# Kernel tuning notes

Measured on AMD Instinct MI355X. Metric: run time of the kernel, lower is better.

Reference implementation:

```python
import jax, jax.numpy as jnp
import numpy as np

VOCAB = 32000
EMB = 256
HID = 512
BATCH = 32
MAXLEN = 64
START_TOKEN = 0


def setup_inputs() -> dict:
    key = jax.random.key(0)
    ks = jax.random.split(key, 10)
    return {
        "encoder_outputs": jax.random.normal(ks[0], (BATCH, 64, HID), dtype=jnp.float32),
        "encoder_hidden": jax.random.normal(ks[1], (1, BATCH, HID), dtype=jnp.float32),
        "target_tensor": jax.random.randint(ks[2], (BATCH, MAXLEN), 0, VOCAB),
        "embedding": jax.random.normal(ks[3], (VOCAB, EMB), dtype=jnp.float32) * 0.02,
        "W_ih": jax.random.normal(ks[4], (3 * HID, EMB), dtype=jnp.float32) * 0.05,
        "W_hh": jax.random.normal(ks[5], (3 * HID, HID), dtype=jnp.float32) * 0.05,
        "b_ih": jax.random.normal(ks[6], (3 * HID,), dtype=jnp.float32) * 0.05,
        "b_hh": jax.random.normal(ks[7], (3 * HID,), dtype=jnp.float32) * 0.05,
        "W_out": jax.random.normal(ks[8], (VOCAB, HID), dtype=jnp.float32) * 0.05,
        "b_out": jax.random.normal(ks[9], (VOCAB,), dtype=jnp.float32) * 0.05,
    }


def _gru_scan(x_seq, h0, W_ih, W_hh, b_ih, b_hh):
    # x_seq: [T, B, E]; h0: [B, H]. torch nn.GRU gate math/order (r, z, n).
    def step(h, x):
        gi = x @ W_ih.T + b_ih            # [B, 3H]
        gh = h @ W_hh.T + b_hh            # [B, 3H]
        i_r, i_z, i_n = jnp.split(gi, 3, axis=-1)
        h_r, h_z, h_n = jnp.split(gh, 3, axis=-1)
        r = jax.nn.sigmoid(i_r + h_r)
        z = jax.nn.sigmoid(i_z + h_z)
        n = jnp.tanh(i_n + r * h_n)
        h_new = (1.0 - z) * n + z * h
        return h_new, h_new
    hT, ys = jax.lax.scan(step, h0, x_seq)
    return ys, hT


def reference(encoder_outputs, encoder_hidden, target_tensor, embedding,
              W_ih, W_hh, b_ih, b_hh, W_out, b_out):
    B = encoder_outputs.shape[0]
    # Teacher forcing: step 0 consumes START, step i consumes target[:, i-1].
    start = jnp.full((B, 1), START_TOKEN, dtype=target_tensor.dtype)
    dec_in = jnp.concatenate([start, target_tensor[:, :-1]], axis=1)  # [B, T]
    # embed -> (dropout p=0 is identity) -> relu
    emb = jax.nn.relu(embedding[dec_in])                # [B, T, E]
    x_seq = jnp.swapaxes(emb, 0, 1)                     # [T, B, E]
    h0 = encoder_hidden[0]                              # [B, H] (num_layers=1)
    ys, hT = _gru_scan(x_seq, h0, W_ih, W_hh, b_ih, b_hh)  # ys: [T, B, H]
    hidden_seq = jnp.swapaxes(ys, 0, 1)                 # [B, T, H]
    logits = jnp.einsum("bth,vh->btv", hidden_seq, W_out) + b_out  # [B, T, V]
    log_probs = jax.nn.log_softmax(logits, axis=-1)
    decoder_hidden = hT[None]                           # [1, B, H]
    return log_probs, decoder_hidden
```

## Files before the change

### kernel.cpp

```cpp
#include <hip/hip_runtime.h>
#include <hip/hip_bf16.h>
#include <math.h>


typedef __bf16 bf16x8 __attribute__((ext_vector_type(8)));
typedef float  f32x4  __attribute__((ext_vector_type(4)));
typedef unsigned short u16;
typedef u16 u16x8v __attribute__((ext_vector_type(8)));
typedef u16 u16x4v __attribute__((ext_vector_type(4)));

#define BTV (32L * 64 * 32000)

#define OFF_X    (0L)
#define SZ_X     (2048L * 256 * 2)
#define OFF_WIH  (OFF_X + SZ_X)
#define SZ_WIH   (1536L * 256 * 2)
#define OFF_WHH  (OFF_WIH + SZ_WIH)
#define SZ_WHH   (1536L * 512 * 2)
#define OFF_WOUT (OFF_WHH + SZ_WHH)
#define SZ_WOUT  (32000L * 512 * 2)
#define OFF_GI   (OFF_WOUT + SZ_WOUT)
#define SZ_GI    (2048L * 1536 * 4)
#define OFF_HS   (OFF_GI + SZ_GI)
#define SZ_HS    (2048L * 512 * 2)
#define OFF_HB   (OFF_HS + SZ_HS)
#define SZ_HB    (2L * 32 * 512 * 2)
#define OFF_FLG  (OFF_HB + SZ_HB)
#define SZ_FLG   (512L)
#define OFF_EV   (OFF_FLG + SZ_FLG)
#define SZ_EV    (64L)
#define WS_NEED  (OFF_EV + SZ_EV)
#define OFF_LG   (WS_NEED + 4096 - (WS_NEED % 4096))
#define SZ_LG    (2048L * 32000 * 2)
#define WS_BIG   (OFF_LG + SZ_LG)

__device__ __forceinline__ u16 f2bf(float f) {
  union { float f; unsigned u; } a; a.f = f;
  unsigned r = a.u + 0x7fffu + ((a.u >> 16) & 1u);
  return (u16)(r >> 16);
}

__device__ __forceinline__ float bf2f(u16 u) {
  union { unsigned u; float f; } a; a.u = ((unsigned)u) << 16;
  return a.f;
}

__device__ __forceinline__ void gload16(const void* g, void* l) {
  __builtin_amdgcn_global_load_lds(
      (const __attribute__((address_space(1))) unsigned int*)g,
      (__attribute__((address_space(3))) unsigned int*)l, 16, 0, 0);
}

extern "C" __global__ void k_cast(const float* __restrict__ s, u16* __restrict__ d, int n4) {
  int i = blockIdx.x * blockDim.x + threadIdx.x;
  int st = gridDim.x * blockDim.x;
  for (; i < n4; i += st) {
    float4 v = reinterpret_cast<const float4*>(s)[i];
    u16x4v o; o.x = f2bf(v.x); o.y = f2bf(v.y); o.z = f2bf(v.z); o.w = f2bf(v.w);
    reinterpret_cast<u16x4v*>(d)[i] = o;
  }
}

extern "C" __global__ void k_embed(const float* __restrict__ emb, const int* __restrict__ tgt,
                                   u16* __restrict__ X) {
  int idx = blockIdx.x * 256 + threadIdx.x;
  int row = idx >> 5;
  int c8  = (idx & 31) << 3;
  int t = row >> 5, b = row & 31;
  int token = (t == 0) ? 0 : tgt[b * 64 + t - 1];
  const float* e = emb + (long)token * 256 + c8;
  u16x8v o;
#pragma unroll
  for (int i = 0; i < 8; ++i) { float v = e[i]; o[i] = f2bf(v > 0.f ? v : 0.f); }
  *reinterpret_cast<u16x8v*>(X + (long)row * 256 + c8) = o;
}

extern "C" __global__ void k_init(unsigned* flags, unsigned* evars) {
  int i = threadIdx.x;
  if (i < 128) {
    unsigned z = 0u;
    asm volatile("global_store_dword %0, %1, off sc0 sc1"
                 :: "v"(flags + i), "v"(z) : "memory");
  }
  if (i < 10) atomicExch(&evars[i], i == 8 ? 0xFFFFFFFFu : 0u);
}

template <bool BF16OUT>
__global__ void __launch_bounds__(256)
k_gemm_t(const u16* __restrict__ A, const u16* __restrict__ B,
         const float* __restrict__ bias, float* __restrict__ C,
         u16* __restrict__ C2, int M, int N, int K) {
  __shared__ u16 At[128 * 32];
  __shared__ u16 Bt[128 * 32];
  int mt = M >> 7;
  int bn = blockIdx.x / mt, bm = blockIdx.x % mt;
  int tid = threadIdx.x, wave = tid >> 6, lane = tid & 63;
  int wr = wave >> 1, wc = wave & 1;
  f32x4 acc[4][4] = {};
  const u16* ga = A + (long)(bm * 128 + wave * 32 + (lane >> 2)) * K + ((lane & 3) << 3);
  const u16* gb = B + (long)(bn * 128 + wave * 32 + (lane >> 2)) * K + ((lane & 3) << 3);
  u16* la0 = &At[wave * 1024]; u16* la1 = la0 + 512;
  u16* lb0 = &Bt[wave * 1024]; u16* lb1 = lb0 + 512;
  long k16 = 16L * K;
  for (int k0 = 0; k0 < K; k0 += 32) {
    if (k0) __syncthreads();
    gload16(ga + k0, la0);
    gload16(ga + k16 + k0, la1);
    gload16(gb + k0, lb0);
    gload16(gb + k16 + k0, lb1);
    __syncthreads();
    bf16x8 af[4], bfr[4];
#pragma unroll
    for (int mi = 0; mi < 4; ++mi)
      af[mi] = *reinterpret_cast<const bf16x8*>(
          &At[(wr * 64 + mi * 16 + (lane & 15)) * 32 + ((lane >> 4) << 3)]);
#pragma unroll
    for (int ni = 0; ni < 4; ++ni)
      bfr[ni] = *reinterpret_cast<const bf16x8*>(
          &Bt[(wc * 64 + ni * 16 + (lane & 15)) * 32 + ((lane >> 4) << 3)]);
#pragma unroll
    for (int mi = 0; mi < 4; ++mi)
#pragma unroll
      for (int ni = 0; ni < 4; ++ni)
        acc[mi][ni] = __builtin_amdgcn_mfma_f32_16x16x32_bf16(af[mi], bfr[ni], acc[mi][ni], 0, 0, 0);
  }
  int rb = bm * 128 + wr * 64 + ((lane >> 4) << 2);
  int cb = bn * 128 + wc * 64 + (lane & 15);
#pragma unroll
  for (int mi = 0; mi < 4; ++mi)
#pragma unroll
    for (int ni = 0; ni < 4; ++ni) {
      int col = cb + ni * 16;
      float bv = bias[col];
#pragma unroll
      for (int q = 0; q < 4; ++q) {
        int rr = rb + mi * 16 + q;
        if (BF16OUT) C2[(long)rr * N + col] = f2bf(acc[mi][ni][q] + bv);
        else         C[(long)rr * N + col] = acc[mi][ni][q] + bv;
      }
    }
}

extern "C" __global__ void __launch_bounds__(768, 1)
k_gru5(const float* __restrict__ gi, const u16* __restrict__ Whh,
       const float* __restrict__ bhh, const float* __restrict__ eh,
       u16* __restrict__ Hb, u16* __restrict__ HS, float* __restrict__ outH,
       unsigned* flags, unsigned* evars) {
  __shared__ u16 Ah[32 * 512];
  __shared__ float gh[3][32][65];
  __shared__ int role_s;
  int tid = threadIdx.x, wave = tid >> 6, lane = tid & 63;
  if (tid == 0) {
    unsigned xcc;
    asm volatile("s_getreg_b32 %0, hwreg(20, 0, 32)" : "=s"(xcc));
    xcc &= 7u;
    unsigned arr = atomicAdd(&evars[xcc], 1u);
    if (arr == 7u) atomicCAS(&evars[8], 0xFFFFFFFFu, xcc);
    unsigned L = 0xFFFFFFFFu;
    for (int it = 0; it < (1 << 24) && L == 0xFFFFFFFFu; ++it) {
      asm volatile("global_load_dword %0, %1, off sc0 sc1\n\ts_waitcnt vmcnt(0)"
                   : "=v"(L) : "v"(evars + 8) : "memory");
    }
    int role = -1;
    if (L == xcc) {
      unsigned c = atomicAdd(&evars[9], 1u);
      if (c < 8u) role = (int)c;
    }
    role_s = role;
  }
  __syncthreads();
  int g = role_s;
  if (g < 0) return;
  int j0 = g * 64;
  int gate = wave >> 2;
  int uh = (wave >> 1) & 1;
  int sig = wave & 1;
  bf16x8 barr[2][8];
  {
    const u16* wbase = Whh + (long)(gate * 512 + j0 + uh * 32) * 512 + sig * 256;
#pragma unroll
    for (int ut = 0; ut < 2; ++ut)
#pragma unroll
      for (int kt = 0; kt < 8; ++kt)
        barr[ut][kt] = *reinterpret_cast<const bf16x8*>(
            wbase + (long)(ut * 16 + (lane & 15)) * 512 + kt * 32 + ((lane >> 4) << 3));
  }
  float hprev[3] = {0.f, 0.f, 0.f}, bb0[3] = {}, bb1[3] = {}, bb2[3] = {};
#pragma unroll
  for (int s = 0; s < 3; ++s) {
    int o = s * 768 + tid;
    if (o < 2048) {
      int b = o >> 6, u = o & 63, j = j0 + u;
      hprev[s] = eh[b * 512 + j];
      bb0[s] = bhh[j]; bb1[s] = bhh[512 + j]; bb2[s] = bhh[1024 + j];
    }
  }
  for (int t = 0; t < 64; ++t) {
    int cur = t & 1, nxt = cur ^ 1;
    float grv[3] = {}, gzv[3] = {}, gnv[3] = {};
#pragma unroll
    for (int s = 0; s < 3; ++s) {
      int o = s * 768 + tid;
      if (o < 2048) {
        int b = o >> 6, u = o & 63, j = j0 + u;
        const float* gp = gi + ((long)t * 32 + b) * 1536;
        grv[s] = gp[j]; gzv[s] = gp[512 + j]; gnv[s] = gp[1024 + j];
      }
    }
    if (t) {
      if (wave == 0) {
        const unsigned* fp = flags + (lane & 7) * 16;
        unsigned v;
        do {
          asm volatile("global_load_dword %0, %1, off sc0 sc1\n\ts_waitcnt vmcnt(0)"
                       : "=v"(v) : "v"(fp) : "memory");
        } while (!__all((int)(v >= (unsigned)t)));
      }
      __syncthreads();
      if (tid < 512) {
        const char* hsrc = (const char*)(Hb + cur * 16384);
        f32x4 d0, d1, d2, d3;
        const void* p0 = hsrc + (0 * 512 + tid) * 16;
        const void* p1 = hsrc + (1 * 512 + tid) * 16;
        const void* p2 = hsrc + (2 * 512 + tid) * 16;
        const void* p3 = hsrc + (3 * 512 + tid) * 16;
        asm volatile(
            "global_load_dwordx4 %0, %4, off sc0\n\t"
            "global_load_dwordx4 %1, %5, off sc0\n\t"
            "global_load_dwordx4 %2, %6, off sc0\n\t"
            "global_load_dwordx4 %3, %7, off sc0\n\t"
            "s_waitcnt vmcnt(0)"
            : "=v"(d0), "=v"(d1), "=v"(d2), "=v"(d3)
            : "v"(p0), "v"(p1), "v"(p2), "v"(p3)
            : "memory");
#pragma unroll
        for (int l = 0; l < 4; ++l) {
          int n = l * 512 + tid;
          int row = n >> 6, i = n & 63;
          f32x4 d = (l == 0) ? d0 : (l == 1) ? d1 : (l == 2) ? d2 : d3;
          *reinterpret_cast<f32x4*>((char*)Ah + row * 1024 + ((i * 16) ^ ((row & 7) << 4))) = d;
        }
      }
    } else {
      if (tid < 512) {
#pragma unroll
        for (int l = 0; l < 4; ++l) {
          int n = l * 512 + tid;
          int row = n >> 6, i = n & 63;
          const float* p = eh + row * 512 + i * 8;
          float4 aa = *reinterpret_cast<const float4*>(p);
          float4 bb = *reinterpret_cast<const float4*>(p + 4);
          u16x8v o8;
          o8[0] = f2bf(aa.x); o8[1] = f2bf(aa.y); o8[2] = f2bf(aa.z); o8[3] = f2bf(aa.w);
          o8[4] = f2bf(bb.x); o8[5] = f2bf(bb.y); o8[6] = f2bf(bb.z); o8[7] = f2bf(bb.w);
          *reinterpret_cast<u16x8v*>((char*)Ah + row * 1024 + ((i * 16) ^ ((row & 7) << 4))) = o8;
        }
      }
    }
    __syncthreads();
    f32x4 acc[2][2] = {};
    int r15 = lane & 15;
    int cbyte = sig * 512 + ((lane >> 4) << 4);
#pragma unroll
    for (int kt = 0; kt < 8; ++kt) {
      bf16x8 a0 = *reinterpret_cast<const bf16x8*>(
          (const char*)Ah + r15 * 1024 + ((kt * 64 + cbyte) ^ ((r15 & 7) << 4)));
      bf16x8 a1 = *reinterpret_cast<const bf16x8*>(
          (const char*)Ah + (16 + r15) * 1024 + ((kt * 64 + cbyte) ^ ((r15 & 7) << 4)));
#pragma unroll
      for (int ut = 0; ut < 2; ++ut) {
        acc[0][ut] = __builtin_amdgcn_mfma_f32_16x16x32_bf16(a0, barr[ut][kt], acc[0][ut], 0, 0, 0);
        acc[1][ut] = __builtin_amdgcn_mfma_f32_16x16x32_bf16(a1, barr[ut][kt], acc[1][ut], 0, 0, 0);
      }
    }
    int ucol = uh * 32 + r15;
    int brow = (lane >> 4) << 2;
    if (sig == 0) {
#pragma unroll
      for (int q = 0; q < 4; ++q) {
        gh[gate][brow + q][ucol]           = acc[0][0][q];
        gh[gate][brow + q][ucol + 16]      = acc[0][1][q];
        gh[gate][16 + brow + q][ucol]      = acc[1][0][q];
        gh[gate][16 + brow + q][ucol + 16] = acc[1][1][q];
      }
    }
    __syncthreads();
    if (sig == 1) {
#pragma unroll
      for (int q = 0; q < 4; ++q) {
        gh[gate][brow + q][ucol]           += acc[0][0][q];
        gh[gate][brow + q][ucol + 16]      += acc[0][1][q];
        gh[gate][16 + brow + q][ucol]      += acc[1][0][q];
        gh[gate][16 + brow + q][ucol + 16] += acc[1][1][q];
      }
    }
    __syncthreads();
#pragma unroll
    for (int s = 0; s < 3; ++s) {
      int o = s * 768 + tid;
      if (o < 2048) {
        int b = o >> 6, u = o & 63, j = j0 + u;
        float hr = gh[0][b][u] + bb0[s];
        float hz = gh[1][b][u] + bb1[s];
        float hn = gh[2][b][u] + bb2[s];
        float r = 1.f / (1.f + __expf(-(grv[s] + hr)));
        float z = 1.f / (1.f + __expf(-(gzv[s] + hz)));
        float x = gnv[s] + r * hn;
        float ax = fabsf(x), ee = __expf(-2.f * ax);
        float th = (1.f - ee) / (1.f + ee);
        th = x < 0.f ? -th : th;
        float hnew = (1.f - z) * th + z * hprev[s];
        hprev[s] = hnew;
        u16 hb = f2bf(hnew);
        u16* hdst = Hb + nxt * 16384 + b * 512 + j;
        asm volatile("global_store_short %0, %1, off sc0"
                     :: "v"(hdst), "v"((unsigned)hb) : "memory");
        HS[((long)b * 64 + t) * 512 + j] = hb;
        if (t == 63) outH[b * 512 + j] = hnew;
      }
    }
    asm volatile("s_waitcnt vmcnt(0)" ::: "memory");
    __syncthreads();
    if (tid == 0) {
      unsigned ph = (unsigned)(t + 1);
      asm volatile("global_store_dword %0, %1, off sc0 sc1\n\ts_waitcnt vmcnt(0)"
                   :: "v"(flags + g * 16), "v"(ph) : "memory");
    }
  }
}

extern "C" __global__ void __launch_bounds__(512)
k_lsm(float* __restrict__ P) {
  extern __shared__ float sr[];
  __shared__ float red[8];
  long base = (long)blockIdx.x * 32000;
  int tid = threadIdx.x, wave = tid >> 6, lane = tid & 63;
  float mx = -INFINITY;
  for (int i = tid; i < 8000; i += 512) {
    float4 v = reinterpret_cast<const float4*>(P + base)[i];
    reinterpret_cast<float4*>(sr)[i] = v;
    mx = fmaxf(mx, fmaxf(fmaxf(v.x, v.y), fmaxf(v.z, v.w)));
  }
#pragma unroll
  for (int off = 32; off; off >>= 1) mx = fmaxf(mx, __shfl_down(mx, off, 64));
  if (lane == 0) red[wave] = mx;
  __syncthreads();
  if (tid == 0) {
    float m = red[0];
#pragma unroll
    for (int w = 1; w < 8; ++w) m = fmaxf(m, red[w]);
    red[0] = m;
  }
  __syncthreads();
  mx = red[0];
  __syncthreads();
  float sm = 0.f;
  for (int i = tid; i < 8000; i += 512) {
    float4 v = reinterpret_cast<const float4*>(sr)[i];
    sm += __expf(v.x - mx) + __expf(v.y - mx) + __expf(v.z - mx) + __expf(v.w - mx);
  }
#pragma unroll
  for (int off = 32; off; off >>= 1) sm += __shfl_down(sm, off, 64);
  if (lane == 0) red[wave] = sm;
  __syncthreads();
  if (tid == 0) {
    float s = 0.f;
#pragma unroll
    for (int w = 0; w < 8; ++w) s += red[w];
    red[0] = mx + __logf(s);
  }
  __syncthreads();
  float L = red[0];
  for (int i = tid; i < 8000; i += 512) {
    float4 v = reinterpret_cast<const float4*>(sr)[i];
    v.x -= L; v.y -= L; v.z -= L; v.w -= L;
    reinterpret_cast<float4*>(P + base)[i] = v;
  }
}

extern "C" __global__ void __launch_bounds__(512)
k_lsm_b(const u16* __restrict__ LG, float* __restrict__ P) {
  extern __shared__ u16 srb[];
  __shared__ float red[8];
  long base = (long)blockIdx.x * 32000;
  int tid = threadIdx.x, wave = tid >> 6, lane = tid & 63;
  float mx = -INFINITY;
  for (int i = tid; i < 4000; i += 512) {
    u16x8v v = reinterpret_cast<const u16x8v*>(LG + base)[i];
    reinterpret_cast<u16x8v*>(srb)[i] = v;
#pragma unroll
    for (int e = 0; e < 8; ++e) mx = fmaxf(mx, bf2f(v[e]));
  }
#pragma unroll
  for (int off = 32; off; off >>= 1) mx = fmaxf(mx, __shfl_down(mx, off, 64));
  if (lane == 0) red[wave] = mx;
  __syncthreads();
  if (tid == 0) {
    float m = red[0];
#pragma unroll
    for (int w = 1; w < 8; ++w) m = fmaxf(m, red[w]);
    red[0] = m;
  }
  __syncthreads();
  mx = red[0];
  __syncthreads();
  float sm = 0.f;
  for (int i = tid; i < 4000; i += 512) {
    u16x8v v = reinterpret_cast<const u16x8v*>(srb)[i];
#pragma unroll
    for (int e = 0; e < 8; ++e) sm += __expf(bf2f(v[e]) - mx);
  }
#pragma unroll
  for (int off = 32; off; off >>= 1) sm += __shfl_down(sm, off, 64);
  if (lane == 0) red[wave] = sm;
  __syncthreads();
  if (tid == 0) {
    float s = 0.f;
#pragma unroll
    for (int w = 0; w < 8; ++w) s += red[w];
    red[0] = mx + __logf(s);
  }
  __syncthreads();
  float L = red[0];
  for (int i = tid; i < 4000; i += 512) {
    u16x8v v = reinterpret_cast<const u16x8v*>(srb)[i];
    float4 o1, o2;
    o1.x = bf2f(v[0]) - L; o1.y = bf2f(v[1]) - L; o1.z = bf2f(v[2]) - L; o1.w = bf2f(v[3]) - L;
    o2.x = bf2f(v[4]) - L; o2.y = bf2f(v[5]) - L; o2.z = bf2f(v[6]) - L; o2.w = bf2f(v[7]) - L;
    reinterpret_cast<float4*>(P + base + (long)i * 8)[0] = o1;
    reinterpret_cast<float4*>(P + base + (long)i * 8)[1] = o2;
  }
}

extern "C" void kernel_launch(void* const* d_in, const int* in_sizes, int n_in,
                              void* d_out, int out_size, void* d_ws, size_t ws_size,
                              hipStream_t stream) {
  (void)in_sizes; (void)n_in; (void)out_size;
  const float* enc_hid = (const float*)d_in[1];
  const int*   tgt     = (const int*)d_in[2];
  const float* emb     = (const float*)d_in[3];
  const float* W_ih    = (const float*)d_in[4];
  const float* W_hh    = (const float*)d_in[5];
  const float* b_ih    = (const float*)d_in[6];
  const float* b_hh    = (const float*)d_in[7];
  const float* W_out   = (const float*)d_in[8];
  const float* b_out   = (const float*)d_in[9];
  float* out = (float*)d_out;
  char* ws = (char*)d_ws;
  if (ws_size < (size_t)WS_NEED) return;
  bool big = ws_size >= (size_t)WS_BIG;

  u16* X        = (u16*)(ws + OFF_X);
  u16* Wih      = (u16*)(ws + OFF_WIH);
  u16* Whh      = (u16*)(ws + OFF_WHH);
  u16* Wout     = (u16*)(ws + OFF_WOUT);
  float* gi     = (float*)(ws + OFF_GI);
  u16* HS       = (u16*)(ws + OFF_HS);
  u16* Hb       = (u16*)(ws + OFF_HB);
  unsigned* flg = (unsigned*)(ws + OFF_FLG);
  unsigned* ev  = (unsigned*)(ws + OFF_EV);
  u16* LG       = (u16*)(ws + OFF_LG);

  hipFuncSetAttribute(reinterpret_cast<const void*>(k_lsm),
                      hipFuncAttributeMaxDynamicSharedMemorySize, 131072);
  hipFuncSetAttribute(reinterpret_cast<const void*>(k_lsm_b),
                      hipFuncAttributeMaxDynamicSharedMemorySize, 65536);

  k_cast<<<96, 256, 0, stream>>>(W_ih, Wih, 1536 * 256 / 4);
  k_cast<<<192, 256, 0, stream>>>(W_hh, Whh, 1536 * 512 / 4);
  k_cast<<<2048, 256, 0, stream>>>(W_out, Wout, 32000 * 512 / 4);
  k_embed<<<256, 256, 0, stream>>>(emb, tgt, X);
  k_init<<<1, 256, 0, stream>>>(flg, ev);
  k_gemm_t<false><<<(1536 / 128) * (2048 / 128), 256, 0, stream>>>(
      X, Wih, b_ih, gi, nullptr, 2048, 1536, 256);
  k_gru5<<<64, 768, 0, stream>>>(gi, Whh, b_hh, enc_hid, Hb, HS, out + BTV, flg, ev);
  if (big) {
    k_gemm_t<true><<<(32000 / 128) * (2048 / 128), 256, 0, stream>>>(
        HS, Wout, b_out, nullptr, LG, 2048, 32000, 512);
    k_lsm_b<<<2048, 512, 64000, stream>>>(LG, out);
  } else {
    k_gemm_t<false><<<(32000 / 128) * (2048 / 128), 256, 0, stream>>>(
        HS, Wout, b_out, out, nullptr, 2048, 32000, 512);
    k_lsm<<<2048, 512, 128000, stream>>>(out);
  }
}
```

Measured before the change: 464.8 us.

## Streamline GRU recurrence and stage bf16 logits in the output buffer

The GRU kernel now reads the previous hidden state straight from the HS sequence buffer, so it no longer writes a separate double-buffered Hb copy. It keeps the two K-halves of the recurrent product in separate shared slots, which removes one block barrier per step. Gate math now uses exp2, pointers are hoisted out of the step loop, and the final hidden state is written once after the loop. The bf16 logits are staged inside each row of the fp32 output buffer using a 64000 stride, so the bf16 GEMM plus log-softmax path always runs and the fp32 fallback is removed. This relies on each log-softmax block copying its row to shared memory before overwriting it.

```diff
diff --git a/kernel.cpp b/kernel.cpp
--- a/kernel.cpp
+++ b/kernel.cpp
@@ -10,6 +10,7 @@
 typedef u16 u16x4v __attribute__((ext_vector_type(4)));
 
 #define BTV (32L * 64 * 32000)
+#define LDC2 64000L
 
 #define OFF_X    (0L)
 #define SZ_X     (2048L * 256 * 2)
@@ -23,16 +24,11 @@
 #define SZ_GI    (2048L * 1536 * 4)
 #define OFF_HS   (OFF_GI + SZ_GI)
 #define SZ_HS    (2048L * 512 * 2)
-#define OFF_HB   (OFF_HS + SZ_HS)
-#define SZ_HB    (2L * 32 * 512 * 2)
-#define OFF_FLG  (OFF_HB + SZ_HB)
+#define OFF_FLG  (OFF_HS + SZ_HS)
 #define SZ_FLG   (512L)
 #define OFF_EV   (OFF_FLG + SZ_FLG)
 #define SZ_EV    (64L)
 #define WS_NEED  (OFF_EV + SZ_EV)
-#define OFF_LG   (WS_NEED + 4096 - (WS_NEED % 4096))
-#define SZ_LG    (2048L * 32000 * 2)
-#define WS_BIG   (OFF_LG + SZ_LG)
 
 __device__ __forceinline__ u16 f2bf(float f) {
   union { float f; unsigned u; } a; a.f = f;
@@ -89,7 +85,7 @@
 __global__ void __launch_bounds__(256)
 k_gemm_t(const u16* __restrict__ A, const u16* __restrict__ B,
          const float* __restrict__ bias, float* __restrict__ C,
-         u16* __restrict__ C2, int M, int N, int K) {
+         u16* __restrict__ C2, int M, int N, int K, long ldc2) {
   __shared__ u16 At[128 * 32];
   __shared__ u16 Bt[128 * 32];
   int mt = M >> 7;
@@ -135,19 +131,19 @@
 #pragma unroll
       for (int q = 0; q < 4; ++q) {
         int rr = rb + mi * 16 + q;
-        if (BF16OUT) C2[(long)rr * N + col] = f2bf(acc[mi][ni][q] + bv);
+        if (BF16OUT) C2[(long)rr * ldc2 + col] = f2bf(acc[mi][ni][q] + bv);
         else         C[(long)rr * N + col] = acc[mi][ni][q] + bv;
       }
     }
 }
 
 extern "C" __global__ void __launch_bounds__(768, 1)
-k_gru5(const float* __restrict__ gi, const u16* __restrict__ Whh,
+k_gru6(const float* __restrict__ gi, const u16* __restrict__ Whh,
        const float* __restrict__ bhh, const float* __restrict__ eh,
-       u16* __restrict__ Hb, u16* __restrict__ HS, float* __restrict__ outH,
+       u16* __restrict__ HS, float* __restrict__ outH,
        unsigned* flags, unsigned* evars) {
   __shared__ u16 Ah[32 * 512];
-  __shared__ float gh[3][32][65];
+  __shared__ float gh[3][2][32][66];
   __shared__ int role_s;
   int tid = threadIdx.x, wave = tid >> 6, lane = tid & 63;
   if (tid == 0) {
@@ -172,9 +168,7 @@
   int g = role_s;
   if (g < 0) return;
   int j0 = g * 64;
-  int gate = wave >> 2;
-  int uh = (wave >> 1) & 1;
-  int sig = wave & 1;
+  int gate = wave >> 2, uh = (wave >> 1) & 1, sig = wave & 1;
   bf16x8 barr[2][8];
   {
     const u16* wbase = Whh + (long)(gate * 512 + j0 + uh * 32) * 512 + sig * 256;
@@ -185,28 +179,60 @@
         barr[ut][kt] = *reinterpret_cast<const bf16x8*>(
             wbase + (long)(ut * 16 + (lane & 15)) * 512 + kt * 32 + ((lane >> 4) << 3));
   }
-  float hprev[3] = {0.f, 0.f, 0.f}, bb0[3] = {}, bb1[3] = {}, bb2[3] = {};
+  bool act2 = tid < 512;
+  float hprev[3] = {}, bb0[3] = {}, bb1[3] = {}, bb2[3] = {};
+  const float* gp0; const float* gp1; const float* gp2 = nullptr;
+  u16* hs0; u16* hs1; u16* hs2 = nullptr;
+  int b_[3], u_[3];
 #pragma unroll
   for (int s = 0; s < 3; ++s) {
     int o = s * 768 + tid;
     if (o < 2048) {
       int b = o >> 6, u = o & 63, j = j0 + u;
+      b_[s] = b; u_[s] = u;
       hprev[s] = eh[b * 512 + j];
       bb0[s] = bhh[j]; bb1[s] = bhh[512 + j]; bb2[s] = bhh[1024 + j];
-    }
-  }
+    } else { b_[s] = 0; u_[s] = 0; }
+  }
+  gp0 = gi + b_[0] * 1536 + j0 + u_[0];
+  gp1 = gi + b_[1] * 1536 + j0 + u_[1];
+  if (act2) gp2 = gi + b_[2] * 1536 + j0 + u_[2];
+  hs0 = HS + ((long)b_[0] * 64) * 512 + j0 + u_[0];
+  hs1 = HS + ((long)b_[1] * 64) * 512 + j0 + u_[1];
+  if (act2) hs2 = HS + ((long)b_[2] * 64) * 512 + j0 + u_[2];
+  const char* sp0 = nullptr; const char* sp1 = nullptr;
+  const char* sp2 = nullptr; const char* sp3 = nullptr;
+  char* ld0 = nullptr; char* ld1 = nullptr; char* ld2 = nullptr; char* ld3 = nullptr;
+  if (tid < 512) {
+#pragma unroll
+    for (int l = 0; l < 4; ++l) {
+      int n = l * 512 + tid;
+      int row = n >> 6, i = n & 63;
+      const char* sp = (const char*)HS + (long)row * 65536 + i * 16 - 1024;
+      char* ld = (char*)Ah + row * 1024 + ((i * 16) ^ ((row & 7) << 4));
+      if (l == 0) { sp0 = sp; ld0 = ld; } else if (l == 1) { sp1 = sp; ld1 = ld; }
+      else if (l == 2) { sp2 = sp; ld2 = ld; } else { sp3 = sp; ld3 = ld; }
+    }
+#pragma unroll
+    for (int l = 0; l < 4; ++l) {
+      int n = l * 512 + tid;
+      int row = n >> 6, i = n & 63;
+      const float* p = eh + row * 512 + i * 8;
+      float4 aa = *reinterpret_cast<const float4*>(p);
+      float4 bb = *reinterpret_cast<const float4*>(p + 4);
+      u16x8v o8;
+      o8[0] = f2bf(aa.x); o8[1] = f2bf(aa.y); o8[2] = f2bf(aa.z); o8[3] = f2bf(aa.w);
+      o8[4] = f2bf(bb.x); o8[5] = f2bf(bb.y); o8[6] = f2bf(bb.z); o8[7] = f2bf(bb.w);
+      *reinterpret_cast<u16x8v*>((char*)Ah + row * 1024 + ((i * 16) ^ ((row & 7) << 4))) = o8;
+    }
+  }
+  const float K1 = -1.44269504f, K2 = 2.88539009f;
   for (int t = 0; t < 64; ++t) {
-    int cur = t & 1, nxt = cur ^ 1;
-    float grv[3] = {}, gzv[3] = {}, gnv[3] = {};
-#pragma unroll
-    for (int s = 0; s < 3; ++s) {
-      int o = s * 768 + tid;
-      if (o < 2048) {
-        int b = o >> 6, u = o & 63, j = j0 + u;
-        const float* gp = gi + ((long)t * 32 + b) * 1536;
-        grv[s] = gp[j]; gzv[s] = gp[512 + j]; gnv[s] = gp[1024 + j];
-      }
-    }
+    float gr0 = gp0[0], gz0 = gp0[512], gn0 = gp0[1024];
+    float gr1 = gp1[0], gz1 = gp1[512], gn1 = gp1[1024];
+    float gr2 = 0.f, gz2 = 0.f, gn2 = 0.f;
+    if (act2) { gr2 = gp2[0]; gz2 = gp2[512]; gn2 = gp2[1024]; }
+    gp0 += 49152; gp1 += 49152; if (act2) gp2 += 49152;
     if (t) {
       if (wave == 0) {
         const unsigned* fp = flags + (lane & 7) * 16;
@@ -218,12 +244,7 @@
       }
       __syncthreads();
       if (tid < 512) {
-        const char* hsrc = (const char*)(Hb + cur * 16384);
         f32x4 d0, d1, d2, d3;
-        const void* p0 = hsrc + (0 * 512 + tid) * 16;
-        const void* p1 = hsrc + (1 * 512 + tid) * 16;
-        const void* p2 = hsrc + (2 * 512 + tid) * 16;
-        const void* p3 = hsrc + (3 * 512 + tid) * 16;
         asm volatile(
             "global_load_dwordx4 %0, %4, off sc0\n\t"
             "global_load_dwordx4 %1, %5, off sc0\n\t"
@@ -231,32 +252,15 @@
             "global_load_dwordx4 %3, %7, off sc0\n\t"
             "s_waitcnt vmcnt(0)"
             : "=v"(d0), "=v"(d1), "=v"(d2), "=v"(d3)
-            : "v"(p0), "v"(p1), "v"(p2), "v"(p3)
+            : "v"(sp0), "v"(sp1), "v"(sp2), "v"(sp3)
             : "memory");
-#pragma unroll
-        for (int l = 0; l < 4; ++l) {
-          int n = l * 512 + tid;
-          int row = n >> 6, i = n & 63;
-          f32x4 d = (l == 0) ? d0 : (l == 1) ? d1 : (l == 2) ? d2 : d3;
-          *reinterpret_cast<f32x4*>((char*)Ah + row * 1024 + ((i * 16) ^ ((row & 7) << 4))) = d;
-        }
+        *reinterpret_cast<f32x4*>(ld0) = d0;
+        *reinterpret_cast<f32x4*>(ld1) = d1;
+        *reinterpret_cast<f32x4*>(ld2) = d2;
+        *reinterpret_cast<f32x4*>(ld3) = d3;
       }
-    } else {
-      if (tid < 512) {
-#pragma unroll
-        for (int l = 0; l < 4; ++l) {
-          int n = l * 512 + tid;
-          int row = n >> 6, i = n & 63;
-          const float* p = eh + row * 512 + i * 8;
-          float4 aa = *reinterpret_cast<const float4*>(p);
-          float4 bb = *reinterpret_cast<const float4*>(p + 4);
-          u16x8v o8;
-          o8[0] = f2bf(aa.x); o8[1] = f2bf(aa.y); o8[2] = f2bf(aa.z); o8[3] = f2bf(aa.w);
-          o8[4] = f2bf(bb.x); o8[5] = f2bf(bb.y); o8[6] = f2bf(bb.z); o8[7] = f2bf(bb.w);
-          *reinterpret_cast<u16x8v*>((char*)Ah + row * 1024 + ((i * 16) ^ ((row & 7) << 4))) = o8;
-        }
-      }
-    }
+    }
+    if (tid < 512) { sp0 += 1024; sp1 += 1024; sp2 += 1024; sp3 += 1024; }
     __syncthreads();
     f32x4 acc[2][2] = {};
     int r15 = lane & 15;
@@ -273,52 +277,40 @@
         acc[1][ut] = __builtin_amdgcn_mfma_f32_16x16x32_bf16(a1, barr[ut][kt], acc[1][ut], 0, 0, 0);
       }
     }
-    int ucol = uh * 32 + r15;
-    int brow = (lane >> 4) << 2;
-    if (sig == 0) {
+    {
+      int ucol = uh * 32 + r15;
+      int brow = (lane >> 4) << 2;
 #pragma unroll
       for (int q = 0; q < 4; ++q) {
-        gh[gate][brow + q][ucol]           = acc[0][0][q];
-        gh[gate][brow + q][ucol + 16]      = acc[0][1][q];
-        gh[gate][16 + brow + q][ucol]      = acc[1][0][q];
-        gh[gate][16 + brow + q][ucol + 16] = acc[1][1][q];
+        gh[gate][sig][brow + q][ucol]           = acc[0][0][q];
+        gh[gate][sig][brow + q][ucol + 16]      = acc[0][1][q];
+        gh[gate][sig][16 + brow + q][ucol]      = acc[1][0][q];
+        gh[gate][sig][16 + brow + q][ucol + 16] = acc[1][1][q];
       }
     }
     __syncthreads();
-    if (sig == 1) {
-#pragma unroll
-      for (int q = 0; q < 4; ++q) {
-        gh[gate][brow + q][ucol]           += acc[0][0][q];
-        gh[gate][brow + q][ucol + 16]      += acc[0][1][q];
-        gh[gate][16 + brow + q][ucol]      += acc[1][0][q];
-        gh[gate][16 + brow + q][ucol + 16] += acc[1][1][q];
-      }
-    }
-    __syncthreads();
 #pragma unroll
     for (int s = 0; s < 3; ++s) {
-      int o = s * 768 + tid;
-      if (o < 2048) {
-        int b = o >> 6, u = o & 63, j = j0 + u;
-        float hr = gh[0][b][u] + bb0[s];
-        float hz = gh[1][b][u] + bb1[s];
-        float hn = gh[2][b][u] + bb2[s];
-        float r = 1.f / (1.f + __expf(-(grv[s] + hr)));
-        float z = 1.f / (1.f + __expf(-(gzv[s] + hz)));
-        float x = gnv[s] + r * hn;
-        float ax = fabsf(x), ee = __expf(-2.f * ax);
-        float th = (1.f - ee) / (1.f + ee);
-        th = x < 0.f ? -th : th;
-        float hnew = (1.f - z) * th + z * hprev[s];
-        hprev[s] = hnew;
-        u16 hb = f2bf(hnew);
-        u16* hdst = Hb + nxt * 16384 + b * 512 + j;
-        asm volatile("global_store_short %0, %1, off sc0"
-                     :: "v"(hdst), "v"((unsigned)hb) : "memory");
-        HS[((long)b * 64 + t) * 512 + j] = hb;
-        if (t == 63) outH[b * 512 + j] = hnew;
-      }
-    }
+      if (s == 2 && !act2) break;
+      int b = b_[s], u = u_[s];
+      float gr = s == 0 ? gr0 : s == 1 ? gr1 : gr2;
+      float gz = s == 0 ? gz0 : s == 1 ? gz1 : gz2;
+      float gn = s == 0 ? gn0 : s == 1 ? gn1 : gn2;
+      float hr = gh[0][0][b][u] + gh[0][1][b][u] + bb0[s];
+      float hz = gh[1][0][b][u] + gh[1][1][b][u] + bb1[s];
+      float hn = gh[2][0][b][u] + gh[2][1][b][u] + bb2[s];
+      float r = 1.f / (1.f + __builtin_amdgcn_exp2f(K1 * (gr + hr)));
+      float z = 1.f / (1.f + __builtin_amdgcn_exp2f(K1 * (gz + hz)));
+      float x = gn + r * hn;
+      float th = 1.f - 2.f / (1.f + __builtin_amdgcn_exp2f(K2 * x));
+      float hnew = th + z * (hprev[s] - th);
+      hprev[s] = hnew;
+      unsigned hb = (unsigned)f2bf(hnew);
+      u16* hp = s == 0 ? hs0 : s == 1 ? hs1 : hs2;
+      asm volatile("global_store_short %0, %1, off sc0"
+                   :: "v"(hp), "v"(hb) : "memory");
+    }
+    hs0 += 512; hs1 += 512; if (act2) hs2 += 512;
     asm volatile("s_waitcnt vmcnt(0)" ::: "memory");
     __syncthreads();
     if (tid == 0) {
@@ -327,66 +319,23 @@
                    :: "v"(flags + g * 16), "v"(ph) : "memory");
     }
   }
+#pragma unroll
+  for (int s = 0; s < 3; ++s) {
+    if (s == 2 && !act2) break;
+    outH[b_[s] * 512 + j0 + u_[s]] = hprev[s];
+  }
 }
 
 extern "C" __global__ void __launch_bounds__(512)
-k_lsm(float* __restrict__ P) {
-  extern __shared__ float sr[];
-  __shared__ float red[8];
-  long base = (long)blockIdx.x * 32000;
-  int tid = threadIdx.x, wave = tid >> 6, lane = tid & 63;
-  float mx = -INFINITY;
-  for (int i = tid; i < 8000; i += 512) {
-    float4 v = reinterpret_cast<const float4*>(P + base)[i];
-    reinterpret_cast<float4*>(sr)[i] = v;
-    mx = fmaxf(mx, fmaxf(fmaxf(v.x, v.y), fmaxf(v.z, v.w)));
-  }
-#pragma unroll
-  for (int off = 32; off; off >>= 1) mx = fmaxf(mx, __shfl_down(mx, off, 64));
-  if (lane == 0) red[wave] = mx;
-  __syncthreads();
-  if (tid == 0) {
-    float m = red[0];
-#pragma unroll
-    for (int w = 1; w < 8; ++w) m = fmaxf(m, red[w]);
-    red[0] = m;
-  }
-  __syncthreads();
-  mx = red[0];
-  __syncthreads();
-  float sm = 0.f;
-  for (int i = tid; i < 8000; i += 512) {
-    float4 v = reinterpret_cast<const float4*>(sr)[i];
-    sm += __expf(v.x - mx) + __expf(v.y - mx) + __expf(v.z - mx) + __expf(v.w - mx);
-  }
-#pragma unroll
-  for (int off = 32; off; off >>= 1) sm += __shfl_down(sm, off, 64);
-  if (lane == 0) red[wave] = sm;
-  __syncthreads();
-  if (tid == 0) {
-    float s = 0.f;
-#pragma unroll
-    for (int w = 0; w < 8; ++w) s += red[w];
-    red[0] = mx + __logf(s);
-  }
-  __syncthreads();
-  float L = red[0];
-  for (int i = tid; i < 8000; i += 512) {
-    float4 v = reinterpret_cast<const float4*>(sr)[i];
-    v.x -= L; v.y -= L; v.z -= L; v.w -= L;
-    reinterpret_cast<float4*>(P + base)[i] = v;
-  }
-}
-
-extern "C" __global__ void __launch_bounds__(512)
-k_lsm_b(const u16* __restrict__ LG, float* __restrict__ P) {
+k_lsm_b(const u16* __restrict__ LGbase, float* __restrict__ P) {
   extern __shared__ u16 srb[];
   __shared__ float red[8];
-  long base = (long)blockIdx.x * 32000;
+  const u16* LG = LGbase + (long)blockIdx.x * LDC2;
+  float* out = P + (long)blockIdx.x * 32000;
   int tid = threadIdx.x, wave = tid >> 6, lane = tid & 63;
   float mx = -INFINITY;
   for (int i = tid; i < 4000; i += 512) {
-    u16x8v v = reinterpret_cast<const u16x8v*>(LG + base)[i];
+    u16x8v v = reinterpret_cast<const u16x8v*>(LG)[i];
     reinterpret_cast<u16x8v*>(srb)[i] = v;
 #pragma unroll
     for (int e = 0; e < 8; ++e) mx = fmaxf(mx, bf2f(v[e]));
@@ -427,8 +376,8 @@
     float4 o1, o2;
     o1.x = bf2f(v[0]) - L; o1.y = bf2f(v[1]) - L; o1.z = bf2f(v[2]) - L; o1.w = bf2f(v[3]) - L;
     o2.x = bf2f(v[4]) - L; o2.y = bf2f(v[5]) - L; o2.z = bf2f(v[6]) - L; o2.w = bf2f(v[7]) - L;
-    reinterpret_cast<float4*>(P + base + (long)i * 8)[0] = o1;
-    reinterpret_cast<float4*>(P + base + (long)i * 8)[1] = o2;
+    reinterpret_cast<float4*>(out + (long)i * 8)[0] = o1;
+    reinterpret_cast<float4*>(out + (long)i * 8)[1] = o2;
   }
 }
 
@@ -448,7 +397,6 @@
   float* out = (float*)d_out;
   char* ws = (char*)d_ws;
   if (ws_size < (size_t)WS_NEED) return;
-  bool big = ws_size >= (size_t)WS_BIG;
 
   u16* X        = (u16*)(ws + OFF_X);
   u16* Wih      = (u16*)(ws + OFF_WIH);
@@ -456,13 +404,10 @@
   u16* Wout     = (u16*)(ws + OFF_WOUT);
   float* gi     = (float*)(ws + OFF_GI);
   u16* HS       = (u16*)(ws + OFF_HS);
-  u16* Hb       = (u16*)(ws + OFF_HB);
   unsigned* flg = (unsigned*)(ws + OFF_FLG);
   unsigned* ev  = (unsigned*)(ws + OFF_EV);
-  u16* LG       = (u16*)(ws + OFF_LG);
-
-  hipFuncSetAttribute(reinterpret_cast<const void*>(k_lsm),
-                      hipFuncAttributeMaxDynamicSharedMemorySize, 131072);
+  u16* LG       = (u16*)d_out;
+
   hipFuncSetAttribute(reinterpret_cast<const void*>(k_lsm_b),
                       hipFuncAttributeMaxDynamicSharedMemorySize, 65536);
 
@@ -472,15 +417,9 @@
   k_embed<<<256, 256, 0, stream>>>(emb, tgt, X);
   k_init<<<1, 256, 0, stream>>>(flg, ev);
   k_gemm_t<false><<<(1536 / 128) * (2048 / 128), 256, 0, stream>>>(
-      X, Wih, b_ih, gi, nullptr, 2048, 1536, 256);
-  k_gru5<<<64, 768, 0, stream>>>(gi, Whh, b_hh, enc_hid, Hb, HS, out + BTV, flg, ev);
-  if (big) {
-    k_gemm_t<true><<<(32000 / 128) * (2048 / 128), 256, 0, stream>>>(
-        HS, Wout, b_out, nullptr, LG, 2048, 32000, 512);
-    k_lsm_b<<<2048, 512, 64000, stream>>>(LG, out);
-  } else {
-    k_gemm_t<false><<<(32000 / 128) * (2048 / 128), 256, 0, stream>>>(
-        HS, Wout, b_out, out, nullptr, 2048, 32000, 512);
-    k_lsm<<<2048, 512, 128000, stream>>>(out);
-  }
-}
+      X, Wih, b_ih, gi, nullptr, 2048, 1536, 256, 0);
+  k_gru6<<<64, 768, 0, stream>>>(gi, Whh, b_hh, enc_hid, HS, out + BTV, flg, ev);
+  k_gemm_t<true><<<(32000 / 128) * (2048 / 128), 256, 0, stream>>>(
+      HS, Wout, b_out, nullptr, LG, 2048, 32000, 512, LDC2);
+  k_lsm_b<<<2048, 512, 64000, stream>>>(LG, out);
+}
```

After: 450.3 us. 3.1% less time.
